# Kernel tuning notes

Hardware: AMD Instinct MI355X
Metric: run time of the kernel (lower is better)

Reference implementation:

```python
import jax, jax.numpy as jnp
import numpy as np

VAR_EPS = 1e-6
N, HID = 100000, 512
D, PH = 64, 16  # input_size, prep_hidden
NOBS = 50000


def setup_inputs() -> dict:
    key = jax.random.key(0)
    ks = jax.random.split(key, 10)
    std = np.sqrt(2.0 / (4 + PH))
    k_gru = 1.0 / np.sqrt(HID)
    inp = {
        "h": jax.random.normal(ks[0], (N, HID), jnp.float32),
        "p": jax.random.normal(ks[1], (N, 2 * D), jnp.float32),
        "X_obs": jax.random.normal(ks[2], (NOBS, D), jnp.float32),
        "M_obs": (jax.random.uniform(ks[3], (NOBS, D)) < 0.5).astype(jnp.float32),
        "i_obs": jnp.sort(jax.random.randint(ks[4], (NOBS,), 0, N)),
        "w_prep": std * jax.random.normal(ks[5], (D, 4, PH), jnp.float32),
        "bias_prep": 0.1 + jnp.zeros((D, PH), jnp.float32),
        "weight_ih": jax.random.uniform(ks[6], (3 * HID, PH * D), jnp.float32, -k_gru, k_gru),
        "weight_hh": jax.random.uniform(ks[7], (3 * HID, HID), jnp.float32, -k_gru, k_gru),
        "bias_ih": jax.random.uniform(ks[8], (3 * HID,), jnp.float32, -k_gru, k_gru),
        "bias_hh": jax.random.uniform(ks[9], (3 * HID,), jnp.float32, -k_gru, k_gru),
    }
    return inp


def _gru_cell(x, hprev, Wih, Whh, bih, bhh):
    gi = x @ Wih.T + bih            # [n, 3H]
    gh = hprev @ Whh.T + bhh        # [n, 3H]
    ir, iz, inn = jnp.split(gi, 3, axis=1)
    hr, hz, hn = jnp.split(gh, 3, axis=1)
    r = jax.nn.sigmoid(ir + hr)
    z = jax.nn.sigmoid(iz + hz)
    n = jnp.tanh(inn + r * hn)
    return (1.0 - z) * n + z * hprev


def reference(h, p, X_obs, M_obs, i_obs, w_prep, bias_prep, weight_ih, weight_hh, bias_ih, bias_hh):
    p_obs = p[i_obs]                              # [n, 2D] gather
    mean, var = jnp.split(p_obs, 2, axis=1)
    var = jnp.abs(var) + VAR_EPS
    error = (X_obs - mean) / jnp.sqrt(var)
    loss = 0.5 * jnp.sum((error * error + jnp.log(var)) * M_obs)

    feats = jnp.stack([X_obs, mean, var, error], axis=2)   # [n, D, 4]
    gru_in = jnp.einsum('ndf,dfp->ndp', feats, w_prep) + bias_prep  # [n, D, PH]
    gru_in = jax.nn.relu(gru_in) * M_obs[:, :, None]
    gru_in = gru_in.reshape(-1, D * PH)

    h_obs_new = _gru_cell(gru_in, h[i_obs], weight_ih, weight_hh, bias_ih, bias_hh)
    h_new = h.at[i_obs].set(h_obs_new)
    return h_new, loss
```

## Files before the change

### kernel.cpp

```cpp
#include <hip/hip_runtime.h>
#include <math.h>

#define NHID 512
typedef unsigned short u16;
typedef __attribute__((ext_vector_type(8))) short short8;
typedef __attribute__((ext_vector_type(16))) float floatx16;

__device__ __forceinline__ unsigned f2b1(float f) {
  unsigned u = __float_as_uint(f);
  return (u + 0x7FFFu + ((u >> 16) & 1u)) >> 16;
}
__device__ __forceinline__ unsigned pk2(float a, float b) {
  return f2b1(a) | (f2b1(b) << 16);
}
__device__ __forceinline__ float sigf(float x) { return 1.0f / (1.0f + expf(-x)); }

__global__ void wtransform(const float* __restrict__ W, uint4* __restrict__ Wt,
                           int Kw, int nch) {
  int u = blockIdx.x * 256 + threadIdx.x;
  int total = 8 * 3 * nch * 512;
  if (u >= total) return;
  int col = u & 63;
  int g8 = (u >> 6) & 7;
  int ch = (u >> 9) % nch;
  int t3 = (u >> 9) / nch;
  int g = t3 % 3, cbb = t3 / 3;
  const float* src = W + (size_t)(g * 512 + cbb * 64 + col) * Kw + ch * 64 + g8 * 8;
  float4 f0 = *(const float4*)src;
  float4 f1 = *(const float4*)(src + 4);
  uint4 v = {pk2(f0.x, f0.y), pk2(f0.z, f0.w), pk2(f1.x, f1.y), pk2(f1.z, f1.w)};
  Wt[u] = v;
}

__global__ void prep_kernel(const float* __restrict__ p,
                            const float* __restrict__ X,
                            const float* __restrict__ Mm,
                            const int* __restrict__ iobs,
                            const float* __restrict__ wprep,
                            const float* __restrict__ bprep,
                            const float* __restrict__ h,
                            u16* __restrict__ A_in, u16* __restrict__ A_h,
                            int* __restrict__ map_i, int* __restrict__ counter,
                            float* __restrict__ partials, int nobs)
{
  __shared__ float sw[4096];
  __shared__ float sb[1024];
  __shared__ int s_cnt[4];
  __shared__ float s_loss[4];
  for (int t = threadIdx.x; t < 4096; t += 256) sw[t] = wprep[t];
  for (int t = threadIdx.x; t < 1024; t += 256) sb[t] = bprep[t];

  const int tid = threadIdx.x;
  const int wave = tid >> 6;
  const int d = tid & 63;
  const int j = blockIdx.x * 4 + wave;
  const bool act = j < nobs;

  int i = 0; bool lastf = false;
  float x = 0.f, mean = 0.f, var = 1.f, m = 0.f, err = 0.f, lossp = 0.f;
  if (act) {
    i = iobs[j];
    lastf = (j == nobs - 1) || (iobs[j + 1] != i);
    mean = p[(size_t)i * 128 + d];
    var  = fabsf(p[(size_t)i * 128 + 64 + d]) + 1e-6f;
    x = X[(size_t)j * 64 + d];
    m = Mm[(size_t)j * 64 + d];
    err = (x - mean) * rsqrtf(var);
    lossp = 0.5f * (err * err + logf(var)) * m;
  }
  __syncthreads();

  #pragma unroll
  for (int off = 32; off > 0; off >>= 1) lossp += __shfl_down(lossp, off, 64);
  if (d == 0) { s_loss[wave] = lossp; s_cnt[wave] = (act && lastf) ? 1 : 0; }
  __syncthreads();
  if (tid == 0) {
    int c0 = s_cnt[0], c1 = s_cnt[1], c2 = s_cnt[2], c3 = s_cnt[3];
    int tot = c0 + c1 + c2 + c3;
    int base = tot ? atomicAdd(counter, tot) : 0;
    s_cnt[0] = base; s_cnt[1] = base + c0;
    s_cnt[2] = base + c0 + c1; s_cnt[3] = base + c0 + c1 + c2;
    partials[blockIdx.x] = s_loss[0] + s_loss[1] + s_loss[2] + s_loss[3];
  }
  __syncthreads();

  if (act && lastf) {
    const int slot = s_cnt[wave];
    if (d == 0) map_i[slot] = i;
    const float* w = sw + d * 64;
    const float* b = sb + d * 16;
    float gi[16];
    #pragma unroll
    for (int ph = 0; ph < 16; ++ph) {
      float v = x * w[ph] + mean * w[16 + ph] + var * w[32 + ph] + err * w[48 + ph] + b[ph];
      gi[ph] = fmaxf(v, 0.0f) * m;
    }
    uint4* dst = (uint4*)(A_in + (size_t)slot * 1024 + d * 16);
    uint4 v0 = {pk2(gi[0], gi[1]), pk2(gi[2], gi[3]), pk2(gi[4], gi[5]), pk2(gi[6], gi[7])};
    uint4 v1 = {pk2(gi[8], gi[9]), pk2(gi[10], gi[11]), pk2(gi[12], gi[13]), pk2(gi[14], gi[15])};
    dst[0] = v0; dst[1] = v1;
    const float4* hp = (const float4*)(h + (size_t)i * NHID + d * 8);
    float4 a = hp[0], bb = hp[1];
    uint4 hv = {pk2(a.x, a.y), pk2(a.z, a.w), pk2(bb.x, bb.y), pk2(bb.z, bb.w)};
    *(uint4*)(A_h + (size_t)slot * 512 + d * 8) = hv;
  }
}

__global__ void loss_sum(const float* __restrict__ partials, int n,
                         float* __restrict__ loss) {
  float s = 0.f;
  for (int t = threadIdx.x; t < n; t += 256) s += partials[t];
  #pragma unroll
  for (int off = 32; off > 0; off >>= 1) s += __shfl_down(s, off, 64);
  __shared__ float sw4[4];
  if ((threadIdx.x & 63) == 0) sw4[threadIdx.x >> 6] = s;
  __syncthreads();
  if (threadIdx.x == 0) loss[0] = sw4[0] + sw4[1] + sw4[2] + sw4[3];
}

__global__ __launch_bounds__(256, 4) void gemm_mfma(
    const u16* __restrict__ A_in, const u16* __restrict__ A_h,
    const uint4* __restrict__ Wt_ih, const uint4* __restrict__ Wt_hh,
    const int* __restrict__ map_i, const int* __restrict__ counter,
    const float* __restrict__ h,
    const float* __restrict__ bih, const float* __restrict__ bhh,
    float* __restrict__ out)
{
  const int ndist = *counter;
  const int j0 = blockIdx.y * 64;
  if (j0 >= ndist) return;
  const int cb = blockIdx.x;
  const int tid = threadIdx.x;
  const int lane = tid & 63;
  const int wave = tid >> 6;
  const int wrow = wave >> 1, wcol = wave & 1;
  const int l31 = lane & 31, kh = lane >> 5;

  __shared__ uint4 sA[8 * 64];
  __shared__ uint4 sB[3 * 8 * 64];

  floatx16 accR = {}, accZ = {}, accI = {}, accH = {};

#define STAGE(Asrc, Ks, Wt, NCH, ch)                                         \
  {                                                                          \
    _Pragma("unroll") for (int pp = 0; pp < 2; ++pp) {                       \
      int g8 = (tid >> 6) + pp * 4;                                          \
      int row = tid & 63;                                                    \
      int gr = j0 + row; if (gr >= ndist) gr = ndist - 1;                    \
      sA[g8 * 64 + row] =                                                    \
          *(const uint4*)(Asrc + (size_t)gr * Ks + ch * 64 + g8 * 8);        \
    }                                                                        \
    _Pragma("unroll") for (int pp = 0; pp < 6; ++pp) {                       \
      int idx = pp * 256 + tid;                                              \
      int g = idx >> 9, rem = idx & 511;                                     \
      sB[idx] = Wt[(size_t)((cb * 3 + g) * NCH + ch) * 512 + rem];           \
    }                                                                        \
  }

#define KSTEPS(ACC3)                                                         \
  _Pragma("unroll") for (int s = 0; s < 4; ++s) {                            \
    int u = (s * 2 + kh) * 64;                                               \
    uint4 av = sA[u + l31 + 32 * wrow];                                      \
    uint4 b0 = sB[0 * 512 + u + l31 + 32 * wcol];                            \
    uint4 b1 = sB[1 * 512 + u + l31 + 32 * wcol];                            \
    uint4 b2 = sB[2 * 512 + u + l31 + 32 * wcol];                            \
    short8 aF = __builtin_bit_cast(short8, av);                              \
    short8 f0 = __builtin_bit_cast(short8, b0);                              \
    short8 f1 = __builtin_bit_cast(short8, b1);                              \
    short8 f2 = __builtin_bit_cast(short8, b2);                              \
    accR = __builtin_amdgcn_mfma_f32_32x32x16_bf16(aF, f0, accR, 0, 0, 0);   \
    accZ = __builtin_amdgcn_mfma_f32_32x32x16_bf16(aF, f1, accZ, 0, 0, 0);   \
    ACC3 = __builtin_amdgcn_mfma_f32_32x32x16_bf16(aF, f2, ACC3, 0, 0, 0);   \
  }

  for (int ch = 0; ch < 16; ++ch) {
    STAGE(A_in, 1024, Wt_ih, 16, ch)
    __syncthreads();
    KSTEPS(accI)
    __syncthreads();
  }
  for (int ch = 0; ch < 8; ++ch) {
    STAGE(A_h, 512, Wt_hh, 8, ch)
    __syncthreads();
    KSTEPS(accH)
    __syncthreads();
  }

  const int col = cb * 64 + 32 * wcol + l31;
  const float biR = bih[col], biZ = bih[512 + col], biN = bih[1024 + col];
  const float bhR = bhh[col], bhZ = bhh[512 + col], bhN = bhh[1024 + col];
  #pragma unroll
  for (int r = 0; r < 16; ++r) {
    int rowl = (r & 3) + 8 * (r >> 2) + 4 * kh + 32 * wrow;
    int jg = j0 + rowl;
    if (jg >= ndist) continue;
    int i = map_i[jg];
    float hv = h[(size_t)i * NHID + col];
    float rr = sigf(accR[r] + biR + bhR);
    float zz = sigf(accZ[r] + biZ + bhZ);
    float nn = tanhf(accI[r] + biN + rr * (accH[r] + bhN));
    out[(size_t)i * NHID + col] = (1.0f - zz) * nn + zz * hv;
  }
#undef STAGE
#undef KSTEPS
}

extern "C" void kernel_launch(void* const* d_in, const int* in_sizes, int n_in,
                              void* d_out, int out_size, void* d_ws, size_t ws_size,
                              hipStream_t stream) {
  const float* h     = (const float*)d_in[0];
  const float* p     = (const float*)d_in[1];
  const float* X     = (const float*)d_in[2];
  const float* Mm    = (const float*)d_in[3];
  const int*   iobs  = (const int*)d_in[4];
  const float* wprep = (const float*)d_in[5];
  const float* bprep = (const float*)d_in[6];
  const float* Wih   = (const float*)d_in[7];
  const float* Whh   = (const float*)d_in[8];
  const float* bih   = (const float*)d_in[9];
  const float* bhh   = (const float*)d_in[10];

  const int N    = in_sizes[0] / NHID;
  const int nobs = in_sizes[4];
  float* out = (float*)d_out;
  float* loss = out + (size_t)N * NHID;

  char* ws = (char*)d_ws;
  int*   counter  = (int*)ws;
  int*   map_i    = (int*)(ws + 1024);
  float* partials = (float*)(ws + (256 << 10));
  u16*   A_in     = (u16*)(ws + (1 << 20));
  u16*   A_h      = (u16*)((char*)A_in + (size_t)nobs * 2048);
  uint4* Wt_ih    = (uint4*)((char*)A_h + (size_t)nobs * 1024);
  uint4* Wt_hh    = (uint4*)((char*)Wt_ih + (size_t)3145728);

  hipMemcpyAsync(d_out, d_in[0], (size_t)N * NHID * sizeof(float),
                 hipMemcpyDeviceToDevice, stream);
  hipMemsetAsync(counter, 0, 4, stream);

  wtransform<<<768, 256, 0, stream>>>(Wih, Wt_ih, 1024, 16);
  wtransform<<<384, 256, 0, stream>>>(Whh, Wt_hh, 512, 8);

  int nblocks = (nobs + 3) / 4;
  prep_kernel<<<nblocks, 256, 0, stream>>>(p, X, Mm, iobs, wprep, bprep, h,
                                           A_in, A_h, map_i, counter, partials, nobs);
  loss_sum<<<1, 256, 0, stream>>>(partials, nblocks, loss);

  dim3 grid(8, (nobs + 63) / 64);
  gemm_mfma<<<grid, 256, 0, stream>>>(A_in, A_h, Wt_ih, Wt_hh, map_i, counter,
                                      h, bih, bhh, out);
}
```

Measured before the change: 934.8 us.

## Double-buffer GEMM weights via global_load_lds with 128-row tiles and register A

Restructures the GRU GEMM so each block covers 128 rows instead of 64, with each wave keeping two 32-row A fragments in registers loaded directly from global memory. Weight tiles are staged into double-buffered LDS through global_load_lds, with manual vmcnt waits and barriers that overlap the next chunk's loads with the current MFMAs. It also swaps hipMemcpyAsync for a custom copy kernel. The changes aim to raise reuse of B tiles and hide load latency, at the cost of more registers (launch bounds drop to 2) and fragile hand-tuned wait counts.

```diff
diff --git a/kernel.cpp b/kernel.cpp
--- a/kernel.cpp
+++ b/kernel.cpp
@@ -14,6 +14,12 @@
   return f2b1(a) | (f2b1(b) << 16);
 }
 __device__ __forceinline__ float sigf(float x) { return 1.0f / (1.0f + expf(-x)); }
+
+__device__ __forceinline__ void gload16(const uint4* g, uint4* l) {
+  __builtin_amdgcn_global_load_lds(
+      (const __attribute__((address_space(1))) unsigned int*)g,
+      (__attribute__((address_space(3))) unsigned int*)l, 16, 0, 0);
+}
 
 __global__ void wtransform(const float* __restrict__ W, uint4* __restrict__ Wt,
                            int Kw, int nch) {
@@ -30,6 +36,13 @@
   float4 f1 = *(const float4*)(src + 4);
   uint4 v = {pk2(f0.x, f0.y), pk2(f0.z, f0.w), pk2(f1.x, f1.y), pk2(f1.z, f1.w)};
   Wt[u] = v;
+}
+
+__global__ void copy_h(const float4* __restrict__ src, float4* __restrict__ dst,
+                       int n4) {
+  int i = blockIdx.x * 256 + threadIdx.x;
+  int stride = gridDim.x * 256;
+  for (; i < n4; i += stride) dst[i] = src[i];
 }
 
 __global__ void prep_kernel(const float* __restrict__ p,
@@ -118,7 +131,7 @@
   if (threadIdx.x == 0) loss[0] = sw4[0] + sw4[1] + sw4[2] + sw4[3];
 }
 
-__global__ __launch_bounds__(256, 4) void gemm_mfma(
+__global__ __launch_bounds__(256, 2) void gemm_mfma(
     const u16* __restrict__ A_in, const u16* __restrict__ A_h,
     const uint4* __restrict__ Wt_ih, const uint4* __restrict__ Wt_hh,
     const int* __restrict__ map_i, const int* __restrict__ counter,
@@ -127,7 +140,7 @@
     float* __restrict__ out)
 {
   const int ndist = *counter;
-  const int j0 = blockIdx.y * 64;
+  const int j0 = blockIdx.y * 128;
   if (j0 >= ndist) return;
   const int cb = blockIdx.x;
   const int tid = threadIdx.x;
@@ -136,73 +149,110 @@
   const int wrow = wave >> 1, wcol = wave & 1;
   const int l31 = lane & 31, kh = lane >> 5;
 
-  __shared__ uint4 sA[8 * 64];
-  __shared__ uint4 sB[3 * 8 * 64];
-
-  floatx16 accR = {}, accZ = {}, accI = {}, accH = {};
-
-#define STAGE(Asrc, Ks, Wt, NCH, ch)                                         \
-  {                                                                          \
-    _Pragma("unroll") for (int pp = 0; pp < 2; ++pp) {                       \
-      int g8 = (tid >> 6) + pp * 4;                                          \
-      int row = tid & 63;                                                    \
-      int gr = j0 + row; if (gr >= ndist) gr = ndist - 1;                    \
-      sA[g8 * 64 + row] =                                                    \
-          *(const uint4*)(Asrc + (size_t)gr * Ks + ch * 64 + g8 * 8);        \
-    }                                                                        \
-    _Pragma("unroll") for (int pp = 0; pp < 6; ++pp) {                       \
-      int idx = pp * 256 + tid;                                              \
-      int g = idx >> 9, rem = idx & 511;                                     \
-      sB[idx] = Wt[(size_t)((cb * 3 + g) * NCH + ch) * 512 + rem];           \
-    }                                                                        \
-  }
-
-#define KSTEPS(ACC3)                                                         \
-  _Pragma("unroll") for (int s = 0; s < 4; ++s) {                            \
-    int u = (s * 2 + kh) * 64;                                               \
-    uint4 av = sA[u + l31 + 32 * wrow];                                      \
-    uint4 b0 = sB[0 * 512 + u + l31 + 32 * wcol];                            \
-    uint4 b1 = sB[1 * 512 + u + l31 + 32 * wcol];                            \
-    uint4 b2 = sB[2 * 512 + u + l31 + 32 * wcol];                            \
-    short8 aF = __builtin_bit_cast(short8, av);                              \
-    short8 f0 = __builtin_bit_cast(short8, b0);                              \
-    short8 f1 = __builtin_bit_cast(short8, b1);                              \
-    short8 f2 = __builtin_bit_cast(short8, b2);                              \
-    accR = __builtin_amdgcn_mfma_f32_32x32x16_bf16(aF, f0, accR, 0, 0, 0);   \
-    accZ = __builtin_amdgcn_mfma_f32_32x32x16_bf16(aF, f1, accZ, 0, 0, 0);   \
-    ACC3 = __builtin_amdgcn_mfma_f32_32x32x16_bf16(aF, f2, ACC3, 0, 0, 0);   \
-  }
-
-  for (int ch = 0; ch < 16; ++ch) {
-    STAGE(A_in, 1024, Wt_ih, 16, ch)
-    __syncthreads();
-    KSTEPS(accI)
-    __syncthreads();
-  }
-  for (int ch = 0; ch < 8; ++ch) {
-    STAGE(A_h, 512, Wt_hh, 8, ch)
-    __syncthreads();
-    KSTEPS(accH)
-    __syncthreads();
-  }
-
-  const int col = cb * 64 + 32 * wcol + l31;
+  __shared__ uint4 sB[2 * 1536];
+
+  floatx16 aR0 = {}, aR1 = {}, aZ0 = {}, aZ1 = {};
+  floatx16 aI0 = {}, aI1 = {}, aH0 = {}, aH1 = {};
+
+  int gr0 = j0 + wrow * 64 + l31;
+  int gr1 = gr0 + 32;
+  if (gr0 >= ndist) gr0 = ndist - 1;
+  if (gr1 >= ndist) gr1 = ndist - 1;
+
+  uint4 aC0[4], aC1[4], aN0[4], aN1[4];
+
+#define STAGE(CH)                                                             \
+  {                                                                           \
+    const uint4* Wt; int nch, cl;                                             \
+    if ((CH) < 16) { Wt = Wt_ih; nch = 16; cl = (CH); }                       \
+    else           { Wt = Wt_hh; nch = 8;  cl = (CH) - 16; }                  \
+    uint4* dst = sB + ((CH) & 1) * 1536;                                      \
+    _Pragma("unroll") for (int pp = 0; pp < 6; ++pp) {                        \
+      int idx = pp * 256 + tid;                                               \
+      int g = idx >> 9, rem = idx & 511;                                      \
+      gload16(Wt + ((size_t)((cb * 3 + g) * nch + cl) << 9) + rem, dst + idx);\
+    }                                                                         \
+  }
+
+#define ALOAD(CH, R0, R1)                                                     \
+  {                                                                           \
+    const u16* Ab; int Ks, cl;                                                \
+    if ((CH) < 16) { Ab = A_in; Ks = 1024; cl = (CH); }                       \
+    else           { Ab = A_h; Ks = 512;  cl = (CH) - 16; }                   \
+    const u16* p0 = Ab + (size_t)gr0 * Ks + cl * 64 + kh * 8;                 \
+    const u16* p1 = Ab + (size_t)gr1 * Ks + cl * 64 + kh * 8;                 \
+    _Pragma("unroll") for (int s = 0; s < 4; ++s) {                           \
+      R0[s] = *(const uint4*)(p0 + s * 16);                                   \
+      R1[s] = *(const uint4*)(p1 + s * 16);                                   \
+    }                                                                         \
+  }
+
+#define KSTEPS(N0, N1)                                                        \
+  _Pragma("unroll") for (int s = 0; s < 4; ++s) {                             \
+    int u = (s * 2 + kh) * 64 + wcol * 32 + l31;                              \
+    uint4 b0 = sBc[u], b1 = sBc[512 + u], b2 = sBc[1024 + u];                 \
+    short8 f0 = __builtin_bit_cast(short8, b0);                               \
+    short8 f1 = __builtin_bit_cast(short8, b1);                               \
+    short8 f2 = __builtin_bit_cast(short8, b2);                               \
+    short8 x0 = __builtin_bit_cast(short8, aC0[s]);                           \
+    short8 x1 = __builtin_bit_cast(short8, aC1[s]);                           \
+    aR0 = __builtin_amdgcn_mfma_f32_32x32x16_bf16(x0, f0, aR0, 0, 0, 0);      \
+    aR1 = __builtin_amdgcn_mfma_f32_32x32x16_bf16(x1, f0, aR1, 0, 0, 0);      \
+    aZ0 = __builtin_amdgcn_mfma_f32_32x32x16_bf16(x0, f1, aZ0, 0, 0, 0);      \
+    aZ1 = __builtin_amdgcn_mfma_f32_32x32x16_bf16(x1, f1, aZ1, 0, 0, 0);      \
+    N0  = __builtin_amdgcn_mfma_f32_32x32x16_bf16(x0, f2, N0, 0, 0, 0);       \
+    N1  = __builtin_amdgcn_mfma_f32_32x32x16_bf16(x1, f2, N1, 0, 0, 0);       \
+  }
+
+  ALOAD(0, aC0, aC1)
+  STAGE(0)
+
+  for (int ch = 0; ch < 24; ++ch) {
+    if (ch < 23) STAGE(ch + 1)
+    if (ch == 0)       asm volatile("s_waitcnt vmcnt(6)" ::: "memory");
+    else if (ch == 23) asm volatile("s_waitcnt vmcnt(8)" ::: "memory");
+    else               asm volatile("s_waitcnt vmcnt(14)" ::: "memory");
+    __builtin_amdgcn_s_barrier();
+    asm volatile("" ::: "memory");
+
+    if (ch < 23) ALOAD(ch + 1, aN0, aN1)
+
+    const uint4* sBc = sB + (ch & 1) * 1536;
+    if (ch < 16) { KSTEPS(aI0, aI1) } else { KSTEPS(aH0, aH1) }
+
+    asm volatile("" ::: "memory");
+    __builtin_amdgcn_s_barrier();
+    if (ch < 23) {
+      #pragma unroll
+      for (int s = 0; s < 4; ++s) { aC0[s] = aN0[s]; aC1[s] = aN1[s]; }
+    }
+  }
+
+  const int col = cb * 64 + wcol * 32 + l31;
   const float biR = bih[col], biZ = bih[512 + col], biN = bih[1024 + col];
   const float bhR = bhh[col], bhZ = bhh[512 + col], bhN = bhh[1024 + col];
-  #pragma unroll
-  for (int r = 0; r < 16; ++r) {
-    int rowl = (r & 3) + 8 * (r >> 2) + 4 * kh + 32 * wrow;
-    int jg = j0 + rowl;
-    if (jg >= ndist) continue;
-    int i = map_i[jg];
-    float hv = h[(size_t)i * NHID + col];
-    float rr = sigf(accR[r] + biR + bhR);
-    float zz = sigf(accZ[r] + biZ + bhZ);
-    float nn = tanhf(accI[r] + biN + rr * (accH[r] + bhN));
-    out[(size_t)i * NHID + col] = (1.0f - zz) * nn + zz * hv;
-  }
+
+#define EPI(R, Z, I, H, RBASE)                                                \
+  _Pragma("unroll") for (int r = 0; r < 16; ++r) {                            \
+    int rowl = (r & 3) + 8 * (r >> 2) + 4 * kh;                               \
+    int jg = (RBASE) + rowl;                                                  \
+    if (jg < ndist) {                                                         \
+      int i = map_i[jg];                                                      \
+      float hv = h[(size_t)i * NHID + col];                                   \
+      float rr = sigf(R[r] + biR + bhR);                                      \
+      float zz = sigf(Z[r] + biZ + bhZ);                                      \
+      float nn = tanhf(I[r] + biN + rr * (H[r] + bhN));                       \
+      out[(size_t)i * NHID + col] = (1.0f - zz) * nn + zz * hv;               \
+    }                                                                         \
+  }
+
+  EPI(aR0, aZ0, aI0, aH0, j0 + wrow * 64)
+  EPI(aR1, aZ1, aI1, aH1, j0 + wrow * 64 + 32)
+
 #undef STAGE
+#undef ALOAD
 #undef KSTEPS
+#undef EPI
 }
 
 extern "C" void kernel_launch(void* const* d_in, const int* in_sizes, int n_in,
@@ -234,9 +284,9 @@
   uint4* Wt_ih    = (uint4*)((char*)A_h + (size_t)nobs * 1024);
   uint4* Wt_hh    = (uint4*)((char*)Wt_ih + (size_t)3145728);
 
-  hipMemcpyAsync(d_out, d_in[0], (size_t)N * NHID * sizeof(float),
-                 hipMemcpyDeviceToDevice, stream);
   hipMemsetAsync(counter, 0, 4, stream);
+
+  copy_h<<<2048, 256, 0, stream>>>((const float4*)h, (float4*)out, N * 128);
 
   wtransform<<<768, 256, 0, stream>>>(Wih, Wt_ih, 1024, 16);
   wtransform<<<384, 256, 0, stream>>>(Whh, Wt_hh, 512, 8);
@@ -246,7 +296,7 @@
                                            A_in, A_h, map_i, counter, partials, nobs);
   loss_sum<<<1, 256, 0, stream>>>(partials, nblocks, loss);
 
-  dim3 grid(8, (nobs + 63) / 64);
+  dim3 grid(8, (nobs + 127) / 128);
   gemm_mfma<<<grid, 256, 0, stream>>>(A_in, A_h, Wt_ih, Wt_hh, map_i, counter,
                                       h, bih, bhh, out);
 }
```

After: 2.363 ms. 153% more time.

## Double-buffer A via direct global-to-LDS loads, stream weights from registers, swizzle grid

Applied to the files above, without the earlier changes.

The GEMM now loads activation tiles straight into double-buffered LDS with global_load_lds, issuing the next chunk's load before computing the current one. Weight fragments are read directly from global memory into registers instead of being staged through LDS. The 1D grid is swizzled so that groups of 8 row blocks share the same column block, which should improve L2 reuse. The launch bound drops to 2 blocks per SM, and the hipMemcpy of h is replaced by a custom copy kernel. The hand-written vmcnt waits depend on exact instruction counts, so a different schedule from the compiler could break correctness or force stalls.

```diff
diff --git a/kernel.cpp b/kernel.cpp
--- a/kernel.cpp
+++ b/kernel.cpp
@@ -14,6 +14,12 @@
   return f2b1(a) | (f2b1(b) << 16);
 }
 __device__ __forceinline__ float sigf(float x) { return 1.0f / (1.0f + expf(-x)); }
+
+__device__ __forceinline__ void gload16(const void* g, void* l) {
+  __builtin_amdgcn_global_load_lds(
+      (const __attribute__((address_space(1))) unsigned int*)g,
+      (__attribute__((address_space(3))) unsigned int*)l, 16, 0, 0);
+}
 
 __global__ void wtransform(const float* __restrict__ W, uint4* __restrict__ Wt,
                            int Kw, int nch) {
@@ -30,6 +36,13 @@
   float4 f1 = *(const float4*)(src + 4);
   uint4 v = {pk2(f0.x, f0.y), pk2(f0.z, f0.w), pk2(f1.x, f1.y), pk2(f1.z, f1.w)};
   Wt[u] = v;
+}
+
+__global__ void copy_h(const float4* __restrict__ src, float4* __restrict__ dst,
+                       int n4) {
+  int i = blockIdx.x * 256 + threadIdx.x;
+  int stride = gridDim.x * 256;
+  for (; i < n4; i += stride) dst[i] = src[i];
 }
 
 __global__ void prep_kernel(const float* __restrict__ p,
@@ -118,7 +131,7 @@
   if (threadIdx.x == 0) loss[0] = sw4[0] + sw4[1] + sw4[2] + sw4[3];
 }
 
-__global__ __launch_bounds__(256, 4) void gemm_mfma(
+__global__ __launch_bounds__(256, 2) void gemm_mfma(
     const u16* __restrict__ A_in, const u16* __restrict__ A_h,
     const uint4* __restrict__ Wt_ih, const uint4* __restrict__ Wt_hh,
     const int* __restrict__ map_i, const int* __restrict__ counter,
@@ -127,64 +140,77 @@
     float* __restrict__ out)
 {
   const int ndist = *counter;
-  const int j0 = blockIdx.y * 64;
+  const int bid = blockIdx.x;
+  const int jb = (bid & 7) + 8 * (bid >> 6);
+  const int cb = (bid >> 3) & 7;
+  const int j0 = jb * 64;
   if (j0 >= ndist) return;
-  const int cb = blockIdx.x;
+
   const int tid = threadIdx.x;
   const int lane = tid & 63;
   const int wave = tid >> 6;
   const int wrow = wave >> 1, wcol = wave & 1;
   const int l31 = lane & 31, kh = lane >> 5;
-
-  __shared__ uint4 sA[8 * 64];
-  __shared__ uint4 sB[3 * 8 * 64];
+  const int arow = l31 + 32 * wrow;
+  const int bcol = l31 + 32 * wcol;
+
+  __shared__ uint4 sA[2 * 512];
 
   floatx16 accR = {}, accZ = {}, accI = {}, accH = {};
 
-#define STAGE(Asrc, Ks, Wt, NCH, ch)                                         \
-  {                                                                          \
-    _Pragma("unroll") for (int pp = 0; pp < 2; ++pp) {                       \
-      int g8 = (tid >> 6) + pp * 4;                                          \
-      int row = tid & 63;                                                    \
-      int gr = j0 + row; if (gr >= ndist) gr = ndist - 1;                    \
-      sA[g8 * 64 + row] =                                                    \
-          *(const uint4*)(Asrc + (size_t)gr * Ks + ch * 64 + g8 * 8);        \
-    }                                                                        \
-    _Pragma("unroll") for (int pp = 0; pp < 6; ++pp) {                       \
-      int idx = pp * 256 + tid;                                              \
-      int g = idx >> 9, rem = idx & 511;                                     \
-      sB[idx] = Wt[(size_t)((cb * 3 + g) * NCH + ch) * 512 + rem];           \
-    }                                                                        \
-  }
-
-#define KSTEPS(ACC3)                                                         \
-  _Pragma("unroll") for (int s = 0; s < 4; ++s) {                            \
-    int u = (s * 2 + kh) * 64;                                               \
-    uint4 av = sA[u + l31 + 32 * wrow];                                      \
-    uint4 b0 = sB[0 * 512 + u + l31 + 32 * wcol];                            \
-    uint4 b1 = sB[1 * 512 + u + l31 + 32 * wcol];                            \
-    uint4 b2 = sB[2 * 512 + u + l31 + 32 * wcol];                            \
-    short8 aF = __builtin_bit_cast(short8, av);                              \
-    short8 f0 = __builtin_bit_cast(short8, b0);                              \
-    short8 f1 = __builtin_bit_cast(short8, b1);                              \
-    short8 f2 = __builtin_bit_cast(short8, b2);                              \
-    accR = __builtin_amdgcn_mfma_f32_32x32x16_bf16(aF, f0, accR, 0, 0, 0);   \
-    accZ = __builtin_amdgcn_mfma_f32_32x32x16_bf16(aF, f1, accZ, 0, 0, 0);   \
-    ACC3 = __builtin_amdgcn_mfma_f32_32x32x16_bf16(aF, f2, ACC3, 0, 0, 0);   \
-  }
-
-  for (int ch = 0; ch < 16; ++ch) {
-    STAGE(A_in, 1024, Wt_ih, 16, ch)
-    __syncthreads();
-    KSTEPS(accI)
-    __syncthreads();
-  }
-  for (int ch = 0; ch < 8; ++ch) {
-    STAGE(A_h, 512, Wt_hh, 8, ch)
-    __syncthreads();
-    KSTEPS(accH)
-    __syncthreads();
-  }
+  int grs = j0 + lane;
+  if (grs >= ndist) grs = ndist - 1;
+
+#define STAGE(CH)                                                             \
+  {                                                                           \
+    const u16* Ab; int Ks, cl;                                                \
+    if ((CH) < 16) { Ab = A_in; Ks = 1024; cl = (CH); }                       \
+    else           { Ab = A_h;  Ks = 512;  cl = (CH) - 16; }                  \
+    _Pragma("unroll") for (int pp = 0; pp < 2; ++pp) {                        \
+      int g8 = wave + pp * 4;                                                 \
+      gload16(Ab + (size_t)grs * Ks + cl * 64 + g8 * 8,                       \
+              sA + ((CH) & 1) * 512 + g8 * 64);                               \
+    }                                                                         \
+  }
+
+#define CHUNK(CH, ACC3, LAST)                                                 \
+  {                                                                           \
+    const uint4* Bp; size_t gs;                                               \
+    if ((CH) < 16) { Bp = Wt_ih + ((size_t)(cb * 3) * 16 + (CH)) * 512;       \
+                     gs = 16 * 512; }                                         \
+    else           { Bp = Wt_hh + ((size_t)(cb * 3) * 8 + (CH) - 16) * 512;   \
+                     gs = 8 * 512; }                                          \
+    uint4 b0[4], b1[4], b2[4];                                                \
+    _Pragma("unroll") for (int s = 0; s < 4; ++s) {                           \
+      int u = (s * 2 + kh) * 64 + bcol;                                       \
+      b0[s] = Bp[u]; b1[s] = Bp[gs + u]; b2[s] = Bp[2 * gs + u];              \
+    }                                                                         \
+    if (!(LAST)) { STAGE((CH) + 1) }                                          \
+    if (!(LAST)) asm volatile("s_waitcnt vmcnt(14)" ::: "memory");            \
+    else         asm volatile("s_waitcnt vmcnt(12)" ::: "memory");            \
+    __builtin_amdgcn_s_barrier();                                             \
+    asm volatile("" ::: "memory");                                            \
+    const uint4* sAc = sA + ((CH) & 1) * 512;                                 \
+    uint4 av[4];                                                              \
+    _Pragma("unroll") for (int s = 0; s < 4; ++s)                             \
+      av[s] = sAc[(s * 2 + kh) * 64 + arow];                                  \
+    _Pragma("unroll") for (int s = 0; s < 4; ++s) {                           \
+      short8 aF = __builtin_bit_cast(short8, av[s]);                          \
+      accR = __builtin_amdgcn_mfma_f32_32x32x16_bf16(                         \
+          aF, __builtin_bit_cast(short8, b0[s]), accR, 0, 0, 0);              \
+      accZ = __builtin_amdgcn_mfma_f32_32x32x16_bf16(                         \
+          aF, __builtin_bit_cast(short8, b1[s]), accZ, 0, 0, 0);              \
+      ACC3 = __builtin_amdgcn_mfma_f32_32x32x16_bf16(                         \
+          aF, __builtin_bit_cast(short8, b2[s]), ACC3, 0, 0, 0);              \
+    }                                                                         \
+    asm volatile("" ::: "memory");                                            \
+    __builtin_amdgcn_s_barrier();                                             \
+  }
+
+  STAGE(0)
+
+  for (int ch = 0; ch < 16; ++ch) { CHUNK(ch, accI, 0) }
+  for (int ch = 16; ch < 24; ++ch) { CHUNK(ch, accH, (ch == 23)) }
 
   const int col = cb * 64 + 32 * wcol + l31;
   const float biR = bih[col], biZ = bih[512 + col], biN = bih[1024 + col];
@@ -202,7 +228,7 @@
     out[(size_t)i * NHID + col] = (1.0f - zz) * nn + zz * hv;
   }
 #undef STAGE
-#undef KSTEPS
+#undef CHUNK
 }
 
 extern "C" void kernel_launch(void* const* d_in, const int* in_sizes, int n_in,
@@ -234,9 +260,9 @@
   uint4* Wt_ih    = (uint4*)((char*)A_h + (size_t)nobs * 1024);
   uint4* Wt_hh    = (uint4*)((char*)Wt_ih + (size_t)3145728);
 
-  hipMemcpyAsync(d_out, d_in[0], (size_t)N * NHID * sizeof(float),
-                 hipMemcpyDeviceToDevice, stream);
   hipMemsetAsync(counter, 0, 4, stream);
+
+  copy_h<<<2048, 256, 0, stream>>>((const float4*)h, (float4*)out, N * 128);
 
   wtransform<<<768, 256, 0, stream>>>(Wih, Wt_ih, 1024, 16);
   wtransform<<<384, 256, 0, stream>>>(Whh, Wt_hh, 512, 8);
@@ -246,7 +272,8 @@
                                            A_in, A_h, map_i, counter, partials, nobs);
   loss_sum<<<1, 256, 0, stream>>>(partials, nblocks, loss);
 
-  dim3 grid(8, (nobs + 63) / 64);
-  gemm_mfma<<<grid, 256, 0, stream>>>(A_in, A_h, Wt_ih, Wt_hh, map_i, counter,
-                                      h, bih, bhh, out);
-}
+  int njb = (nobs + 63) / 64;
+  int nhi = (njb + 7) / 8;
+  gemm_mfma<<<64 * nhi, 256, 0, stream>>>(A_in, A_h, Wt_ih, Wt_hh, map_i,
+                                          counter, h, bih, bhh, out);
+}
```

New measurement: 938.7 us. Within noise of the previous version (+0.4%).
